# Optimization experiments

Hardware: AMD Instinct MI355X
Metric: run time of the kernel (lower is better)

## Reference

```python
import jax, jax.numpy as jnp
import numpy as np

B, S, DIM = 4, 2048, 512
HEADS, DHEAD = 8, 64
INNER = HEADS * DHEAD


def setup_inputs() -> dict:
    key = jax.random.key(0)
    k1, k2, k3, k4 = jax.random.split(key, 4)
    x = jax.random.normal(k1, (B, S, DIM), dtype=jnp.float32)
    W_qkv = jax.random.normal(k2, (DIM, 3 * INNER), dtype=jnp.float32) * (DIM ** -0.5)
    W_out = jax.random.normal(k3, (INNER, DIM), dtype=jnp.float32) * (INNER ** -0.5)
    b_out = jnp.zeros((DIM,), dtype=jnp.float32)
    # learnable log-temperature, initialized to log(dim_head**-0.5)
    log_temp = jnp.asarray(np.log(DHEAD ** -0.5), dtype=jnp.float32)
    return {"x": x, "W_qkv": W_qkv, "log_temp": log_temp, "W_out": W_out, "b_out": b_out}


def reference(x, W_qkv, log_temp, W_out, b_out):
    b, s, _ = x.shape
    qkv = x @ W_qkv  # [b, s, 3*inner]
    q, k, v = jnp.split(qkv, 3, axis=-1)
    # [b, s, inner] -> [b, h, s, d]
    reshape = lambda t: t.reshape(b, s, HEADS, DHEAD).transpose(0, 2, 1, 3)
    q, k, v = reshape(q), reshape(k), reshape(v)
    dots = jnp.einsum("bhid,bhjd->bhij", q, k) * jnp.exp(log_temp)
    mask_value = -jnp.finfo(dots.dtype).max
    eye = jnp.eye(s, dtype=bool)
    dots = jnp.where(eye, mask_value, dots)
    attn = jax.nn.softmax(dots, axis=-1)
    out = jnp.einsum("bhij,bhjd->bhid", attn, v)
    out = out.transpose(0, 2, 1, 3).reshape(b, s, INNER)
    return out @ W_out + b_out
```

## Files before the change

kernel.cpp:

```cpp
#include <hip/hip_runtime.h>
#include <hip/hip_bf16.h>

#define BB 4
#define SS 2048
#define DIMM 512
#define HH 8
#define DD 64
#define NQKV 1536

typedef float  floatx4 __attribute__((ext_vector_type(4)));
typedef short  bf16x8  __attribute__((ext_vector_type(8)));
typedef short  bf16x4  __attribute__((ext_vector_type(4)));

#define MFMA16(A, B, C) __builtin_amdgcn_mfma_f32_16x16x32_bf16(A, B, C, 0, 0, 0)

__device__ __forceinline__ floatx4 MFMA16K16(bf16x4 a, bf16x4 b, floatx4 c) {
#if __has_builtin(__builtin_amdgcn_mfma_f32_16x16x16bf16_1k)
    return __builtin_amdgcn_mfma_f32_16x16x16bf16_1k(a, b, c, 0, 0, 0);
#else
    floatx4 d;
    asm volatile("v_mfma_f32_16x16x16_bf16 %0, %1, %2, %3"
                 : "=v"(d) : "v"(a), "v"(b), "v"(c));
    return d;
#endif
}

__device__ __forceinline__ unsigned short f2bf(float f) {
    unsigned int u = __float_as_uint(f);
    u += 0x7FFFu + ((u >> 16) & 1u);
    return (unsigned short)(u >> 16);
}

__device__ __forceinline__ unsigned int f2bf_pk(float lo, float hi) {
    float2 f; f.x = lo; f.y = hi;
    __hip_bfloat162 h = __float22bfloat162_rn(f);
    return *reinterpret_cast<unsigned int*>(&h);
}

__device__ __forceinline__ float fast_exp2(float x) {
#if __has_builtin(__builtin_amdgcn_exp2f)
    return __builtin_amdgcn_exp2f(x);
#else
    return __exp2f(x);
#endif
}

__device__ __forceinline__ void gl_lds16(const void* g, void* l) {
    __builtin_amdgcn_global_load_lds(
        (__attribute__((address_space(1))) void*)g,
        (__attribute__((address_space(3))) void*)l,
        16, 0, 0);
}

__global__ __launch_bounds__(256) void k_prep(
    const float* __restrict__ x, const float* __restrict__ W_qkv,
    const float* __restrict__ W_out,
    unsigned short* __restrict__ xb, unsigned short* __restrict__ Wq_t,
    unsigned short* __restrict__ Wo_t) {
    __shared__ float t[32][33];
    int bid = blockIdx.x, tid = threadIdx.x;
    if (bid < 4096) {
        int i = (bid * 256 + tid) * 4;
        float4 v = *(const float4*)(x + i);
        ushort4 o;
        o.x = f2bf(v.x); o.y = f2bf(v.y); o.z = f2bf(v.z); o.w = f2bf(v.w);
        *(ushort4*)(xb + i) = o;
        return;
    }
    const float* in; unsigned short* out; int R = 512, C, bx, by;
    if (bid < 4864) { in = W_qkv; out = Wq_t; C = 1536; int blk = bid - 4096; bx = blk % 48; by = blk / 48; }
    else            { in = W_out; out = Wo_t; C = 512;  int blk = bid - 4864; bx = blk % 16; by = blk / 16; }
    int tx = tid & 31, ty = tid >> 5;
    int c0 = bx * 32, r0 = by * 32;
    for (int i = 0; i < 4; i++) {
        int r = r0 + ty + i * 8;
        t[ty + i * 8][tx] = in[(size_t)r * C + c0 + tx];
    }
    __syncthreads();
    for (int i = 0; i < 4; i++) {
        int cc = c0 + ty + i * 8;
        out[(size_t)cc * R + r0 + tx] = f2bf(t[tx][ty + i * 8]);
    }
}

__global__ __launch_bounds__(256) void k_gemm_qkv(
    const unsigned short* __restrict__ A,
    const unsigned short* __restrict__ Bt,
    const float* __restrict__ log_temp,
    unsigned short* __restrict__ Qb,
    unsigned short* __restrict__ Kb,
    unsigned short* __restrict__ Vt) {
    __shared__ unsigned short smem[2][128 * 64];
    unsigned short* As = smem[0];
    unsigned short* Bs = smem[1];
    const int K = 512;
    int m0 = blockIdx.x * 128, n0 = blockIdx.y * 128;
    int tid = threadIdx.x;
    int w = tid >> 6, lane = tid & 63;
    int c = lane & 15, q4 = lane >> 4;
    int wm = w >> 1, wn = w & 1;
    float qscale = __expf(log_temp[0]) * 1.44269504f;

    floatx4 acc[4][4] = {};

    for (int k0 = 0; k0 < K; k0 += 64) {
        __syncthreads();
        for (int i = 0; i < 4; i++) {
            int cidx = w * 256 + i * 64 + lane;
            int row = cidx >> 3, cc = cidx & 7;
            int gcc = cc ^ (row & 7);
            gl_lds16(A + (size_t)(m0 + row) * K + k0 + gcc * 8,
                     As + (size_t)(w * 256 + i * 64) * 8);
            gl_lds16(Bt + (size_t)(n0 + row) * K + k0 + gcc * 8,
                     Bs + (size_t)(w * 256 + i * 64) * 8);
        }
        __syncthreads();
        bf16x8 aF[2][4], bF[2][4];
        for (int kh = 0; kh < 2; kh++)
            for (int mt = 0; mt < 4; mt++) {
                int row = wm * 64 + mt * 16 + c;
                aF[kh][mt] = *(const bf16x8*)&As[row * 64 + (((kh * 4 + q4) ^ (row & 7)) * 8)];
            }
        for (int kh = 0; kh < 2; kh++)
            for (int nt = 0; nt < 4; nt++) {
                int row = wn * 64 + nt * 16 + c;
                bF[kh][nt] = *(const bf16x8*)&Bs[row * 64 + (((kh * 4 + q4) ^ (row & 7)) * 8)];
            }
        for (int kh = 0; kh < 2; kh++)
            for (int mt = 0; mt < 4; mt++)
                for (int nt = 0; nt < 4; nt++)
                    acc[mt][nt] = MFMA16(aF[kh][mt], bF[kh][nt], acc[mt][nt]);
    }

    if (n0 < 1024) {
        for (int nt = 0; nt < 4; nt++) {
            int n = n0 + wn * 64 + nt * 16 + c;
            int t = n >> 9, inner = n & 511;
            int h = inner >> 6, d = inner & 63;
            for (int mt = 0; mt < 4; mt++) {
                for (int r = 0; r < 4; r++) {
                    int m = m0 + wm * 64 + mt * 16 + q4 * 4 + r;
                    int b = m >> 11, s = m & 2047;
                    int bh = b * 8 + h;
                    float v = acc[mt][nt][r];
                    if (t == 0)  Qb[((size_t)bh * SS + s) * 64 + d] = f2bf(v * qscale);
                    else         Kb[((size_t)bh * SS + s) * 64 + d] = f2bf(v);
                }
            }
        }
    } else {
        unsigned short* T = &smem[0][0];
        int b = m0 >> 11, s_base = m0 & 2047;
        for (int half = 0; half < 2; half++) {
            __syncthreads();
            if (wn == half) {
                for (int nt = 0; nt < 4; nt++)
                    for (int mt = 0; mt < 4; mt++)
                        for (int r = 0; r < 4; r++)
                            T[(nt * 16 + c) * 136 + wm * 64 + mt * 16 + q4 * 4 + r] =
                                f2bf(acc[mt][nt][r]);
            }
            __syncthreads();
            for (int rr = 0; rr < 4; rr++) {
                int nl = w * 16 + rr * 4 + q4;
                int ml = c * 8;
                bf16x8 v = *(const bf16x8*)&T[nl * 136 + ml];
                int n = n0 + half * 64 + nl;
                int h = (n >> 6) - 16, d = n & 63;
                int bh = b * 8 + h;
                *(bf16x8*)(Vt + ((size_t)bh * 64 + d) * SS + s_base + ml) = v;
            }
        }
    }
}

__global__ __launch_bounds__(512, 4) void k_attn(
    const unsigned short* __restrict__ Qb,
    const unsigned short* __restrict__ Kb,
    const unsigned short* __restrict__ Vt,
    unsigned short* __restrict__ AO) {
    __shared__ unsigned short Ks[2][64 * 64];
    __shared__ unsigned short Vs[2][64 * 64];
    int q0 = blockIdx.x * 128;
    int h = blockIdx.y, b = blockIdx.z;
    int bh = b * 8 + h;
    int tid = threadIdx.x, w = tid >> 6, lane = tid & 63;
    int c = lane & 15, q4 = lane >> 4;

    const unsigned short* Kbase = Kb + (size_t)bh * SS * 64;
    const unsigned short* Vbase = Vt + (size_t)bh * 64 * SS;

    bf16x8 qf[2];
    {
        const unsigned short* qp = Qb + ((size_t)bh * SS + q0 + w * 16 + c) * 64;
        qf[0] = *(const bf16x8*)(qp + q4 * 8);
        qf[1] = *(const bf16x8*)(qp + 32 + q4 * 8);
    }

    int grow = tid >> 3, gcc = (tid & 7) ^ (grow & 7);
    const unsigned short* ksrc = Kbase + (size_t)grow * 64 + gcc * 8;
    const unsigned short* vsrc = Vbase + (size_t)grow * SS + gcc * 8;
    unsigned short* kdst = (unsigned short*)Ks[0] + w * 512;
    unsigned short* vdst = (unsigned short*)Vs[0] + w * 512;

    gl_lds16(ksrc, kdst);
    gl_lds16(vsrc, vdst);

    int mask_j0 = (q0 + w * 16) & ~63;
    int mglob = q0 + w * 16 + c;
    floatx4 oacc[4] = {};
    float psum = 0.f;

    for (int j0 = 0; j0 < SS; j0 += 64) {
        int buf = (j0 >> 6) & 1;
        __syncthreads();
        if (j0 + 64 < SS) {
            gl_lds16(ksrc + (size_t)(j0 + 64) * 64, kdst + (buf ^ 1) * 4096);
            gl_lds16(vsrc + (j0 + 64), vdst + (buf ^ 1) * 4096);
        }
        bool diag = (j0 == mask_j0);

        for (int jt = 0; jt < 4; jt++) {
            int row = jt * 16 + c;
            bf16x8 kf0 = *(const bf16x8*)&Ks[buf][row * 64 + ((q4 ^ (row & 7)) * 8)];
            bf16x8 kf1 = *(const bf16x8*)&Ks[buf][row * 64 + (((4 + q4) ^ (row & 7)) * 8)];
            floatx4 sa = {};
            sa = MFMA16(kf0, qf[0], sa);
            sa = MFMA16(kf1, qf[1], sa);

            if (diag) {
                for (int r = 0; r < 4; r++) {
                    int jg = j0 + jt * 16 + q4 * 4 + r;
                    if (jg == mglob) sa[r] = -1e30f;
                }
            }

            float e0 = fast_exp2(sa[0]), e1 = fast_exp2(sa[1]);
            float e2 = fast_exp2(sa[2]), e3 = fast_exp2(sa[3]);
            psum += (e0 + e1) + (e2 + e3);
            union { bf16x4 v; unsigned int u[2]; } P;
            P.u[0] = f2bf_pk(e0, e1); P.u[1] = f2bf_pk(e2, e3);

            int chunk = jt * 2 + (q4 >> 1);
            int sub = (q4 & 1) * 4;
            for (int dt = 0; dt < 4; dt++) {
                int vrow = dt * 16 + c;
                bf16x4 vf = *(const bf16x4*)&Vs[buf][vrow * 64 + ((chunk ^ (vrow & 7)) * 8) + sub];
                oacc[dt] = MFMA16K16(P.v, vf, oacc[dt]);
            }
        }
    }

    float l = psum;
    l += __shfl_xor(l, 16);
    l += __shfl_xor(l, 32);
    for (int r = 0; r < 4; r++) {
        float lr = __shfl(l, q4 * 4 + r, 64);
        float inv = 1.0f / lr;
        int s = q0 + w * 16 + q4 * 4 + r;
        for (int dt = 0; dt < 4; dt++)
            AO[((size_t)b * SS + s) * 512 + h * 64 + dt * 16 + c] =
                f2bf(oacc[dt][r] * inv);
    }
}

__global__ __launch_bounds__(256) void k_gemm_out(
    const unsigned short* __restrict__ A,
    const unsigned short* __restrict__ Bt,
    const float* __restrict__ bias,
    float* __restrict__ out) {
    __shared__ unsigned short As[64 * 64];
    __shared__ unsigned short Bs[128 * 64];
    const int K = 512;
    int m0 = blockIdx.x * 64, n0 = blockIdx.y * 128;
    int tid = threadIdx.x;
    int w = tid >> 6, lane = tid & 63;
    int c = lane & 15, q4 = lane >> 4;

    floatx4 acc[8] = {};

    for (int k0 = 0; k0 < K; k0 += 64) {
        __syncthreads();
        for (int i = 0; i < 2; i++) {
            int cidx = i * 256 + tid;
            int row = cidx >> 3, cc = cidx & 7;
            int gcc = cc ^ (row & 7);
            gl_lds16(A + (size_t)(m0 + row) * K + k0 + gcc * 8,
                     As + (size_t)(i * 256 + w * 64) * 8);
        }
        for (int i = 0; i < 4; i++) {
            int cidx = i * 256 + tid;
            int row = cidx >> 3, cc = cidx & 7;
            int gcc = cc ^ (row & 7);
            gl_lds16(Bt + (size_t)(n0 + row) * K + k0 + gcc * 8,
                     Bs + (size_t)(i * 256 + w * 64) * 8);
        }
        __syncthreads();
        bf16x8 aF[2], bF[2][8];
        for (int kh = 0; kh < 2; kh++) {
            int row = w * 16 + c;
            aF[kh] = *(const bf16x8*)&As[row * 64 + (((kh * 4 + q4) ^ (row & 7)) * 8)];
        }
        for (int kh = 0; kh < 2; kh++)
            for (int nt = 0; nt < 8; nt++) {
                int row = nt * 16 + c;
                bF[kh][nt] = *(const bf16x8*)&Bs[row * 64 + (((kh * 4 + q4) ^ (row & 7)) * 8)];
            }
        for (int kh = 0; kh < 2; kh++)
            for (int nt = 0; nt < 8; nt++)
                acc[nt] = MFMA16(aF[kh], bF[kh][nt], acc[nt]);
    }

    for (int nt = 0; nt < 8; nt++) {
        int n = n0 + nt * 16 + c;
        float bv = bias[n];
        for (int r = 0; r < 4; r++) {
            int m = m0 + w * 16 + q4 * 4 + r;
            out[(size_t)m * 512 + n] = acc[nt][r] + bv;
        }
    }
}

extern "C" void kernel_launch(void* const* d_in, const int* in_sizes, int n_in,
                              void* d_out, int out_size, void* d_ws, size_t ws_size,
                              hipStream_t stream) {
    const float* x        = (const float*)d_in[0];
    const float* W_qkv    = (const float*)d_in[1];
    const float* log_temp = (const float*)d_in[2];
    const float* W_out    = (const float*)d_in[3];
    const float* b_out    = (const float*)d_in[4];
    float* out = (float*)d_out;

    char* ws = (char*)d_ws;
    unsigned short* xb   = (unsigned short*)(ws + 0);
    unsigned short* Wq_t = (unsigned short*)(ws + 8388608);
    unsigned short* Wo_t = (unsigned short*)(ws + 9961472);
    unsigned short* Qb   = (unsigned short*)(ws + 10485760);
    unsigned short* Kb   = (unsigned short*)(ws + 18874368);
    unsigned short* Vt   = (unsigned short*)(ws + 27262976);
    unsigned short* AO   = (unsigned short*)(ws + 35651584);

    k_prep<<<5120, 256, 0, stream>>>(x, W_qkv, W_out, xb, Wq_t, Wo_t);
    k_gemm_qkv<<<dim3(64, 12), 256, 0, stream>>>(xb, Wq_t, log_temp, Qb, Kb, Vt);
    k_attn<<<dim3(16, 8, 4), 512, 0, stream>>>(Qb, Kb, Vt, AO);
    k_gemm_out<<<dim3(128, 4), 256, 0, stream>>>(AO, Wo_t, b_out, out);
}
```

Measured before the change: 164.7 us.

## Give each attention wave two query tiles and use K32 MFMA for PV

The attention kernel drops from 512 to 256 threads per block, and each wave now handles 32 query rows (two 16-row tiles). Each K and V fragment loaded from LDS is reused across both query tiles. K rows are permuted so a lane's eight P values line up with the 16x16x32 bf16 MFMA, which replaces the 16x16x16 MFMA for P·V and halves the number of PV instructions. The trade-off is more registers per wave (double accumulators) and fewer waves per block to hide latency.

```diff
diff --git a/kernel.cpp b/kernel.cpp
--- a/kernel.cpp
+++ b/kernel.cpp
@@ -13,17 +13,6 @@
 typedef short  bf16x4  __attribute__((ext_vector_type(4)));
 
 #define MFMA16(A, B, C) __builtin_amdgcn_mfma_f32_16x16x32_bf16(A, B, C, 0, 0, 0)
-
-__device__ __forceinline__ floatx4 MFMA16K16(bf16x4 a, bf16x4 b, floatx4 c) {
-#if __has_builtin(__builtin_amdgcn_mfma_f32_16x16x16bf16_1k)
-    return __builtin_amdgcn_mfma_f32_16x16x16bf16_1k(a, b, c, 0, 0, 0);
-#else
-    floatx4 d;
-    asm volatile("v_mfma_f32_16x16x16_bf16 %0, %1, %2, %3"
-                 : "=v"(d) : "v"(a), "v"(b), "v"(c));
-    return d;
-#endif
-}
 
 __device__ __forceinline__ unsigned short f2bf(float f) {
     unsigned int u = __float_as_uint(f);
@@ -174,7 +163,7 @@
     }
 }
 
-__global__ __launch_bounds__(512, 4) void k_attn(
+__global__ __launch_bounds__(256, 4) void k_attn(
     const unsigned short* __restrict__ Qb,
     const unsigned short* __restrict__ Kb,
     const unsigned short* __restrict__ Vt,
@@ -190,77 +179,105 @@
     const unsigned short* Kbase = Kb + (size_t)bh * SS * 64;
     const unsigned short* Vbase = Vt + (size_t)bh * 64 * SS;
 
-    bf16x8 qf[2];
-    {
-        const unsigned short* qp = Qb + ((size_t)bh * SS + q0 + w * 16 + c) * 64;
-        qf[0] = *(const bf16x8*)(qp + q4 * 8);
-        qf[1] = *(const bf16x8*)(qp + 32 + q4 * 8);
-    }
-
-    int grow = tid >> 3, gcc = (tid & 7) ^ (grow & 7);
-    const unsigned short* ksrc = Kbase + (size_t)grow * 64 + gcc * 8;
-    const unsigned short* vsrc = Vbase + (size_t)grow * SS + gcc * 8;
-    unsigned short* kdst = (unsigned short*)Ks[0] + w * 512;
-    unsigned short* vdst = (unsigned short*)Vs[0] + w * 512;
-
-    gl_lds16(ksrc, kdst);
-    gl_lds16(vsrc, vdst);
-
-    int mask_j0 = (q0 + w * 16) & ~63;
-    int mglob = q0 + w * 16 + c;
-    floatx4 oacc[4] = {};
-    float psum = 0.f;
+    bf16x8 qf[2][2];
+    for (int mt = 0; mt < 2; mt++) {
+        const unsigned short* qp = Qb + ((size_t)bh * SS + q0 + w * 32 + mt * 16 + c) * 64;
+        qf[mt][0] = *(const bf16x8*)(qp + q4 * 8);
+        qf[mt][1] = *(const bf16x8*)(qp + 32 + q4 * 8);
+    }
+
+    int cidx0 = w * 128 + lane, cidx1 = cidx0 + 64;
+    int row0 = cidx0 >> 3, cc0 = cidx0 & 7;
+    int row1 = cidx1 >> 3, cc1 = cidx1 & 7;
+    int fk0 = (row0 & 3) | ((row0 >> 1) & 4);
+    int fk1 = (row1 & 3) | ((row1 >> 1) & 4);
+    const unsigned short* ksrc0 = Kbase + (size_t)row0 * 64 + (cc0 ^ fk0) * 8;
+    const unsigned short* ksrc1 = Kbase + (size_t)row1 * 64 + (cc1 ^ fk1) * 8;
+    const unsigned short* vsrc0 = Vbase + (size_t)row0 * SS + (cc0 ^ (row0 & 7)) * 8;
+    const unsigned short* vsrc1 = Vbase + (size_t)row1 * SS + (cc1 ^ (row1 & 7)) * 8;
+    unsigned short* kdst0 = &Ks[0][0] + w * 1024;
+    unsigned short* kdst1 = kdst0 + 512;
+    unsigned short* vdst0 = &Vs[0][0] + w * 1024;
+    unsigned short* vdst1 = vdst0 + 512;
+
+    gl_lds16(ksrc0, kdst0); gl_lds16(ksrc1, kdst1);
+    gl_lds16(vsrc0, vdst0); gl_lds16(vsrc1, vdst1);
+
+    int mask_j0 = (q0 + w * 32) & ~63;
+    int mglob0 = q0 + w * 32 + c;
+    int mglob1 = mglob0 + 16;
+    floatx4 oacc[2][4] = {};
+    float psum[2] = {0.f, 0.f};
 
     for (int j0 = 0; j0 < SS; j0 += 64) {
         int buf = (j0 >> 6) & 1;
         __syncthreads();
         if (j0 + 64 < SS) {
-            gl_lds16(ksrc + (size_t)(j0 + 64) * 64, kdst + (buf ^ 1) * 4096);
-            gl_lds16(vsrc + (j0 + 64), vdst + (buf ^ 1) * 4096);
+            gl_lds16(ksrc0 + (size_t)(j0 + 64) * 64, kdst0 + (buf ^ 1) * 4096);
+            gl_lds16(ksrc1 + (size_t)(j0 + 64) * 64, kdst1 + (buf ^ 1) * 4096);
+            gl_lds16(vsrc0 + (j0 + 64), vdst0 + (buf ^ 1) * 4096);
+            gl_lds16(vsrc1 + (j0 + 64), vdst1 + (buf ^ 1) * 4096);
         }
         bool diag = (j0 == mask_j0);
 
-        for (int jt = 0; jt < 4; jt++) {
-            int row = jt * 16 + c;
-            bf16x8 kf0 = *(const bf16x8*)&Ks[buf][row * 64 + ((q4 ^ (row & 7)) * 8)];
-            bf16x8 kf1 = *(const bf16x8*)&Ks[buf][row * 64 + (((4 + q4) ^ (row & 7)) * 8)];
-            floatx4 sa = {};
-            sa = MFMA16(kf0, qf[0], sa);
-            sa = MFMA16(kf1, qf[1], sa);
-
-            if (diag) {
-                for (int r = 0; r < 4; r++) {
-                    int jg = j0 + jt * 16 + q4 * 4 + r;
-                    if (jg == mglob) sa[r] = -1e30f;
-                }
-            }
-
-            float e0 = fast_exp2(sa[0]), e1 = fast_exp2(sa[1]);
-            float e2 = fast_exp2(sa[2]), e3 = fast_exp2(sa[3]);
-            psum += (e0 + e1) + (e2 + e3);
-            union { bf16x4 v; unsigned int u[2]; } P;
-            P.u[0] = f2bf_pk(e0, e1); P.u[1] = f2bf_pk(e2, e3);
-
-            int chunk = jt * 2 + (q4 >> 1);
-            int sub = (q4 & 1) * 4;
+        for (int g = 0; g < 2; g++) {
+            bf16x8 kf[2][2];
+            for (int inner = 0; inner < 2; inner++) {
+                int row = g * 32 + ((c >> 2) << 3) + inner * 4 + (c & 3);
+                kf[inner][0] = *(const bf16x8*)&Ks[buf][row * 64 + ((q4 ^ (c & 7)) * 8)];
+                kf[inner][1] = *(const bf16x8*)&Ks[buf][row * 64 + (((4 + q4) ^ (c & 7)) * 8)];
+            }
+            bf16x8 vf[4];
             for (int dt = 0; dt < 4; dt++) {
                 int vrow = dt * 16 + c;
-                bf16x4 vf = *(const bf16x4*)&Vs[buf][vrow * 64 + ((chunk ^ (vrow & 7)) * 8) + sub];
-                oacc[dt] = MFMA16K16(P.v, vf, oacc[dt]);
-            }
-        }
-    }
-
-    float l = psum;
-    l += __shfl_xor(l, 16);
-    l += __shfl_xor(l, 32);
-    for (int r = 0; r < 4; r++) {
-        float lr = __shfl(l, q4 * 4 + r, 64);
-        float inv = 1.0f / lr;
-        int s = q0 + w * 16 + q4 * 4 + r;
-        for (int dt = 0; dt < 4; dt++)
-            AO[((size_t)b * SS + s) * 512 + h * 64 + dt * 16 + c] =
-                f2bf(oacc[dt][r] * inv);
+                vf[dt] = *(const bf16x8*)&Vs[buf][vrow * 64 + (((g * 4 + q4) ^ (c & 7)) * 8)];
+            }
+
+            floatx4 sa[2][2];
+            for (int mt = 0; mt < 2; mt++)
+                for (int inner = 0; inner < 2; inner++) {
+                    floatx4 t = {};
+                    t = MFMA16(kf[inner][0], qf[mt][0], t);
+                    t = MFMA16(kf[inner][1], qf[mt][1], t);
+                    sa[mt][inner] = t;
+                }
+
+            if (diag) {
+                for (int inner = 0; inner < 2; inner++)
+                    for (int r = 0; r < 4; r++) {
+                        int jg = j0 + g * 32 + q4 * 8 + inner * 4 + r;
+                        if (jg == mglob0) sa[0][inner][r] = -1e30f;
+                        if (jg == mglob1) sa[1][inner][r] = -1e30f;
+                    }
+            }
+
+            for (int mt = 0; mt < 2; mt++) {
+                float e0 = fast_exp2(sa[mt][0][0]), e1 = fast_exp2(sa[mt][0][1]);
+                float e2 = fast_exp2(sa[mt][0][2]), e3 = fast_exp2(sa[mt][0][3]);
+                float e4 = fast_exp2(sa[mt][1][0]), e5 = fast_exp2(sa[mt][1][1]);
+                float e6 = fast_exp2(sa[mt][1][2]), e7 = fast_exp2(sa[mt][1][3]);
+                psum[mt] += ((e0 + e1) + (e2 + e3)) + ((e4 + e5) + (e6 + e7));
+                union { bf16x8 v; unsigned int u[4]; } P;
+                P.u[0] = f2bf_pk(e0, e1); P.u[1] = f2bf_pk(e2, e3);
+                P.u[2] = f2bf_pk(e4, e5); P.u[3] = f2bf_pk(e6, e7);
+                for (int dt = 0; dt < 4; dt++)
+                    oacc[mt][dt] = MFMA16(P.v, vf[dt], oacc[mt][dt]);
+            }
+        }
+    }
+
+    for (int mt = 0; mt < 2; mt++) {
+        float l = psum[mt];
+        l += __shfl_xor(l, 16);
+        l += __shfl_xor(l, 32);
+        for (int r = 0; r < 4; r++) {
+            float lr = __shfl(l, q4 * 4 + r, 64);
+            float inv = 1.0f / lr;
+            int s = q0 + w * 32 + mt * 16 + q4 * 4 + r;
+            for (int dt = 0; dt < 4; dt++)
+                AO[((size_t)b * SS + s) * 512 + h * 64 + dt * 16 + c] =
+                    f2bf(oacc[mt][dt][r] * inv);
+        }
     }
 }
 
@@ -342,6 +359,6 @@
 
     k_prep<<<5120, 256, 0, stream>>>(x, W_qkv, W_out, xb, Wq_t, Wo_t);
     k_gemm_qkv<<<dim3(64, 12), 256, 0, stream>>>(xb, Wq_t, log_temp, Qb, Kb, Vt);
-    k_attn<<<dim3(16, 8, 4), 512, 0, stream>>>(Qb, Kb, Vt, AO);
+    k_attn<<<dim3(16, 8, 4), 256, 0, stream>>>(Qb, Kb, Vt, AO);
     k_gemm_out<<<dim3(128, 4), 256, 0, stream>>>(AO, Wo_t, b_out, out);
 }
```

New measurement: 156.2 us. 5.2% less time.
